# Performance work log

Hardware: AMD Instinct MI355X
Metric: run time of the kernel (lower is better)

The kernel has to match this reference:

```python
import jax, jax.numpy as jnp
import numpy as np

FACTOR = 2
EPS = 1e-5


def _layernorm_last(x, w, b):
    # LayerNorm over the last dim only (torch nn.LayerNorm(size) with int size)
    mu = jnp.mean(x, axis=-1, keepdims=True)
    var = jnp.var(x, axis=-1, keepdims=True)
    return (x - mu) * jax.lax.rsqrt(var + EPS) * w + b


def setup_inputs() -> dict:
    key = jax.random.key(0)
    ks = jax.random.split(key, 12)
    B, C, H, W = 8, 512, 128, 128
    C8 = C // 8
    S = (H // FACTOR)  # = 64, LayerNorm size
    x = jax.random.normal(ks[0], (B, C, H, W), jnp.float32)
    s = 1.0 / np.sqrt(C)
    wq = jax.random.normal(ks[1], (C8, C), jnp.float32) * s
    bq = jax.random.normal(ks[2], (C8,), jnp.float32) * 0.02
    wk = jax.random.normal(ks[3], (C8, C), jnp.float32) * s
    bk = jax.random.normal(ks[4], (C8,), jnp.float32) * 0.02
    wv = jax.random.normal(ks[5], (C, C), jnp.float32) * s
    bv = jax.random.normal(ks[6], (C,), jnp.float32) * 0.02
    gamma = jax.random.normal(ks[7], (1,), jnp.float32) * 0.1
    ln_in_w = 1.0 + 0.1 * jax.random.normal(ks[8], (S,), jnp.float32)
    ln_in_b = 0.1 * jax.random.normal(ks[9], (S,), jnp.float32)
    ln_out_w = 1.0 + 0.1 * jax.random.normal(ks[10], (S,), jnp.float32)
    ln_out_b = 0.1 * jax.random.normal(ks[11], (S,), jnp.float32)
    return {"x": x, "wq": wq, "bq": bq, "wk": wk, "bk": bk, "wv": wv, "bv": bv,
            "gamma": gamma, "ln_in_w": ln_in_w, "ln_in_b": ln_in_b,
            "ln_out_w": ln_out_w, "ln_out_b": ln_out_b}


def reference(x, wq, bq, wk, bk, wv, bv, gamma, ln_in_w, ln_in_b, ln_out_w, ln_out_b):
    B, C, H, W = x.shape
    f = FACTOR
    Hp, Wp = H // f, W // f
    N = Hp * Wp
    # AvgPool2d(factor)
    xp = x.reshape(B, C, Hp, f, Wp, f).mean(axis=(3, 5))
    # LayerNorm over last dim (width)
    xn = _layernorm_last(xp, ln_in_w, ln_in_b)
    # 1x1 conv projections (einsum over channels)
    q = jnp.einsum('oc,bchw->bohw', wq, xn) + bq[None, :, None, None]
    k = jnp.einsum('oc,bchw->bohw', wk, xn) + bk[None, :, None, None]
    v = jnp.einsum('oc,bchw->bohw', wv, xn) + bv[None, :, None, None]
    q = q.reshape(B, -1, N)  # (B, C/8, N)
    k = k.reshape(B, -1, N)
    v = v.reshape(B, C, N)
    # energy = Q^T K, no scale (as in source)
    energy = jnp.einsum('bcn,bcm->bnm', q, k)  # (B, N, N)
    att = jax.nn.softmax(energy, axis=-1)
    # out = V @ att^T : out[b,c,n] = sum_m v[b,c,m] * att[b,n,m]
    out = jnp.einsum('bcm,bnm->bcn', v, att).reshape(B, C, Hp, Wp)
    out = _layernorm_last(out, ln_out_w, ln_out_b)
    # F.interpolate(scale_factor=f) -> nearest upsample
    out = jnp.repeat(jnp.repeat(out, f, axis=2), f, axis=3)
    return gamma * out + x
```

## Files before the change

kernel.cpp:

```cpp
#include <hip/hip_runtime.h>
#include <hip/hip_bf16.h>
#include <stdint.h>

#define BB 8
#define CC 512
#define HH 128
#define WW 128
#define HP 64
#define NN 4096
#define C8 64
#define EPSF 1e-5f
#define LOG2E 1.4426950408889634f
#define SM_SHIFT 46.0f

typedef __attribute__((ext_vector_type(8))) short short8;
typedef __attribute__((ext_vector_type(4))) float f32x4;

__device__ __forceinline__ float bf2f(ushort u) {
    union { uint i; float f; } x; x.i = ((uint)u) << 16; return x.f;
}
__device__ __forceinline__ ushort f2bf(float f) {
    uint i = __float_as_uint(f);
    return (ushort)((i + 0x7FFFu + ((i >> 16) & 1u)) >> 16);
}
__device__ __forceinline__ uint cvt_pk_bf16(float lo, float hi) {
    uint r;
    asm("v_cvt_pk_bf16_f32 %0, %1, %2" : "=v"(r) : "v"(lo), "v"(hi));
    return r;
}

__global__ __launch_bounds__(256) void pool_ln_kernel(
    const float* __restrict__ x, const float* __restrict__ lw,
    const float* __restrict__ lb, ushort* __restrict__ xn)
{
    int wid = threadIdx.x >> 6, lane = threadIdx.x & 63;
    int row = blockIdx.x * 4 + wid;
    int h = row & 63;
    int bc = row >> 6;
    const float* r0 = x + ((size_t)bc * 128 + 2 * h) * 128;
    const float* r1 = r0 + 128;
    float2 a0 = ((const float2*)r0)[lane];
    float2 a1 = ((const float2*)r1)[lane];
    float p = 0.25f * (a0.x + a0.y + a1.x + a1.y);
    float s = p, sq = p * p;
    #pragma unroll
    for (int m = 1; m < 64; m <<= 1) {
        s  += __shfl_xor(s,  m, 64);
        sq += __shfl_xor(sq, m, 64);
    }
    float mu  = s * (1.f / 64.f);
    float var = sq * (1.f / 64.f) - mu * mu;
    float inv = rsqrtf(var + EPSF);
    float v = (p - mu) * inv * lw[lane] + lb[lane];
    xn[(size_t)bc * NN + h * 64 + lane] = f2bf(v);
}

__global__ __launch_bounds__(256) void qkv_kernel(
    const ushort* __restrict__ xn,
    const float* __restrict__ wq, const float* __restrict__ bq,
    const float* __restrict__ wk, const float* __restrict__ bk,
    const float* __restrict__ wv, const float* __restrict__ bv,
    ushort* __restrict__ qo, ushort* __restrict__ ko, ushort* __restrict__ vo)
{
    __shared__ __align__(16) ushort As[64][40];
    __shared__ __align__(16) ushort Bs[64][66];
    int b = blockIdx.z, mt = blockIdx.y;
    int n0 = blockIdx.x * 64;
    const float* W; const float* bias; ushort* outp;
    if (mt == 0)      { W = wq;                               bias = bq;              outp = qo + (size_t)b * C8 * NN; }
    else if (mt == 1) { W = wk;                               bias = bk;              outp = ko + (size_t)b * C8 * NN; }
    else              { W = wv + (size_t)(mt - 2) * 64 * 512; bias = bv + (mt - 2) * 64;
                        outp = vo + (size_t)b * CC * NN + (size_t)(mt - 2) * 64 * NN; }
    float mult = (mt == 0) ? LOG2E : 1.0f;
    const ushort* xb = xn + (size_t)b * CC * NN;
    int t = threadIdx.x;
    int lane = t & 63, wid = t >> 6;
    int wm = wid >> 1, wn = wid & 1;
    f32x4 acc[2][2] = {};

    for (int kc = 0; kc < 512; kc += 32) {
        {
            int row = t >> 2, k8 = (t & 3) * 8;
            const float* wp_ = &W[row * 512 + kc + k8];
            float4 f0 = *(const float4*)wp_;
            float4 f1 = *(const float4*)(wp_ + 4);
            ushort tmp[8] = { f2bf(f0.x * mult), f2bf(f0.y * mult), f2bf(f0.z * mult), f2bf(f0.w * mult),
                              f2bf(f1.x * mult), f2bf(f1.y * mult), f2bf(f1.z * mult), f2bf(f1.w * mult) };
            *(uint4*)&As[row][k8] = *(const uint4*)tmp;
        }
        {
            int c = t >> 3, n8 = (t & 7) * 8;
            uint4 v = *(const uint4*)&xb[(size_t)(kc + c) * NN + n0 + n8];
            const ushort* pv = (const ushort*)&v;
            #pragma unroll
            for (int e = 0; e < 8; e++) Bs[n8 + e][c] = pv[e];
        }
        __syncthreads();
        short8 a[2];
        #pragma unroll
        for (int fm = 0; fm < 2; fm++)
            a[fm] = *(const short8*)&As[wm * 32 + fm * 16 + (lane & 15)][(lane >> 4) * 8];
        short8 bb[2];
        #pragma unroll
        for (int fn = 0; fn < 2; fn++) {
            int col = wn * 32 + fn * 16 + (lane & 15);
            union { short8 v; uint u[4]; } bu;
            int c0 = (lane >> 4) * 8;
            #pragma unroll
            for (int p = 0; p < 4; p++)
                bu.u[p] = *(const uint*)&Bs[col][c0 + 2 * p];
            bb[fn] = bu.v;
        }
        #pragma unroll
        for (int fm = 0; fm < 2; fm++)
            #pragma unroll
            for (int fn = 0; fn < 2; fn++)
                acc[fm][fn] = __builtin_amdgcn_mfma_f32_16x16x32_bf16(a[fm], bb[fn], acc[fm][fn], 0, 0, 0);
        __syncthreads();
    }
    #pragma unroll
    for (int fm = 0; fm < 2; fm++) {
        #pragma unroll
        for (int fn = 0; fn < 2; fn++) {
            int col = n0 + wn * 32 + fn * 16 + (lane & 15);
            #pragma unroll
            for (int r = 0; r < 4; r++) {
                int orow = wm * 32 + fm * 16 + (lane >> 4) * 4 + r;
                outp[(size_t)orow * NN + col] = f2bf(acc[fm][fn][r] + bias[orow] * mult);
            }
        }
    }
}

__global__ __launch_bounds__(256, 4) void attn_kernel(
    const ushort* __restrict__ qg, const ushort* __restrict__ kg,
    const ushort* __restrict__ vg, const float* __restrict__ x,
    const float* __restrict__ gamma_p,
    const float* __restrict__ lnw_g, const float* __restrict__ lnb_g,
    float* __restrict__ out)
{
    __shared__ __align__(16) ushort KQ[2][4][64][16];
    __shared__ __align__(16) ushort Ps[2][64][72];
    __shared__ float row_l[64];
    __shared__ float lnw[64], lnb[64];

    int bid = blockIdx.x;
    int b  = bid & 7;
    int cq = (bid >> 3) & 3;
    int h  = bid >> 5;
    int t = threadIdx.x, wid = t >> 6, lane = t & 63;
    const ushort* qb = qg + (size_t)b * C8 * NN;
    const ushort* kb = kg + (size_t)b * C8 * NN;
    const ushort* vb = vg + (size_t)b * CC * NN;

    if (t < 64) { lnw[t] = lnw_g[t]; lnb[t] = lnb_g[t]; }

    int sc_ = t >> 2, sm16 = (t & 3) * 16;
    {
        *(uint4*)&KQ[1][t & 3][sc_][0] = *(const uint4*)&qb[(size_t)sc_ * NN + h * 64 + sm16];
        *(uint4*)&KQ[1][t & 3][sc_][8] = *(const uint4*)&qb[(size_t)sc_ * NN + h * 64 + sm16 + 8];
        *(uint4*)&KQ[0][t & 3][sc_][0] = *(const uint4*)&kb[(size_t)sc_ * NN + sm16];
        *(uint4*)&KQ[0][t & 3][sc_][8] = *(const uint4*)&kb[(size_t)sc_ * NN + sm16 + 8];
    }
    __syncthreads();

    uint trofs = 2u * ((uint)(lane & 15) + (((uint)lane >> 4) << 6));

    short8 qf[2];
    {
        uint qaddr = (uint)(uintptr_t)&KQ[1][wid][0][0] + trofs;
        union { short8 v; unsigned long long u[2]; } q0, q1;
        asm volatile("ds_read_b64_tr_b16 %0, %4\n"
                     "ds_read_b64_tr_b16 %1, %4 offset:512\n"
                     "ds_read_b64_tr_b16 %2, %4 offset:1024\n"
                     "ds_read_b64_tr_b16 %3, %4 offset:1536"
                     : "=&v"(q0.u[0]), "=&v"(q0.u[1]), "=&v"(q1.u[0]), "=&v"(q1.u[1])
                     : "v"(qaddr));
        asm volatile("s_waitcnt lgkmcnt(0)" ::: "memory");
        __builtin_amdgcn_sched_barrier(0);
        qf[0] = q0.v; qf[1] = q1.v;
    }
    __syncthreads();

    f32x4 acc[4][2] = {};
    float lsum = 0.f;
    int cbase = cq * 128 + wid * 32;
    int nrow = wid * 16 + (lane & 15);
    int mq4 = (lane >> 4) * 4;

    for (int mt = 0; mt < 64; mt++) {
        int cur = mt & 1, nxt = cur ^ 1;
        int m0 = mt * 64;
        int m0n = ((mt + 1) & 63) * 64;
        uint4 kp0 = *(const uint4*)&kb[(size_t)sc_ * NN + m0n + sm16];
        uint4 kp1 = *(const uint4*)&kb[(size_t)sc_ * NN + m0n + sm16 + 8];

        f32x4 sfT[4];
        #pragma unroll
        for (int fp = 0; fp < 2; fp++) {
            union { short8 v; unsigned long long u[2]; } ka[2], kc2[2];
            uint a0 = (uint)(uintptr_t)&KQ[cur][fp * 2][0][0] + trofs;
            uint a1 = (uint)(uintptr_t)&KQ[cur][fp * 2 + 1][0][0] + trofs;
            asm volatile("ds_read_b64_tr_b16 %0, %4\n"
                         "ds_read_b64_tr_b16 %1, %4 offset:512\n"
                         "ds_read_b64_tr_b16 %2, %4 offset:1024\n"
                         "ds_read_b64_tr_b16 %3, %4 offset:1536"
                         : "=&v"(ka[0].u[0]), "=&v"(ka[0].u[1]), "=&v"(ka[1].u[0]), "=&v"(ka[1].u[1])
                         : "v"(a0));
            asm volatile("ds_read_b64_tr_b16 %0, %4\n"
                         "ds_read_b64_tr_b16 %1, %4 offset:512\n"
                         "ds_read_b64_tr_b16 %2, %4 offset:1024\n"
                         "ds_read_b64_tr_b16 %3, %4 offset:1536"
                         : "=&v"(kc2[0].u[0]), "=&v"(kc2[0].u[1]), "=&v"(kc2[1].u[0]), "=&v"(kc2[1].u[1])
                         : "v"(a1));
            asm volatile("s_waitcnt lgkmcnt(0)" ::: "memory");
            __builtin_amdgcn_sched_barrier(0);
            f32x4 s0 = {}, s1 = {};
            s0 = __builtin_amdgcn_mfma_f32_16x16x32_bf16(ka[0].v,  qf[0], s0, 0, 0, 0);
            s0 = __builtin_amdgcn_mfma_f32_16x16x32_bf16(ka[1].v,  qf[1], s0, 0, 0, 0);
            s1 = __builtin_amdgcn_mfma_f32_16x16x32_bf16(kc2[0].v, qf[0], s1, 0, 0, 0);
            s1 = __builtin_amdgcn_mfma_f32_16x16x32_bf16(kc2[1].v, qf[1], s1, 0, 0, 0);
            sfT[fp * 2] = s0; sfT[fp * 2 + 1] = s1;
        }

        #pragma unroll
        for (int fn = 0; fn < 4; fn++) {
            float e0 = exp2f(sfT[fn][0] - SM_SHIFT);
            float e1 = exp2f(sfT[fn][1] - SM_SHIFT);
            float e2 = exp2f(sfT[fn][2] - SM_SHIFT);
            float e3 = exp2f(sfT[fn][3] - SM_SHIFT);
            lsum += (e0 + e1) + (e2 + e3);
            uint2 pk;
            pk.x = cvt_pk_bf16(e0, e1);
            pk.y = cvt_pk_bf16(e2, e3);
            *(uint2*)&Ps[cur][nrow][fn * 16 + mq4] = pk;
        }

        *(uint4*)&KQ[nxt][t & 3][sc_][0] = kp0;
        *(uint4*)&KQ[nxt][t & 3][sc_][8] = kp1;

        __syncthreads();

        #pragma unroll
        for (int ks = 0; ks < 2; ks++) {
            short8 pb[2];
            #pragma unroll
            for (int g = 0; g < 2; g++)
                pb[g] = *(const short8*)&vb[(size_t)(cbase + g * 16 + (lane & 15)) * NN
                                            + m0 + ks * 32 + (lane >> 4) * 8];
            short8 pa[4];
            #pragma unroll
            for (int f = 0; f < 4; f++)
                pa[f] = *(const short8*)&Ps[cur][f * 16 + (lane & 15)][ks * 32 + (lane >> 4) * 8];
            #pragma unroll
            for (int g = 0; g < 2; g++)
                #pragma unroll
                for (int f = 0; f < 4; f++)
                    acc[f][g] = __builtin_amdgcn_mfma_f32_16x16x32_bf16(pa[f], pb[g], acc[f][g], 0, 0, 0);
        }
    }

    lsum += __shfl_xor(lsum, 16, 64);
    lsum += __shfl_xor(lsum, 32, 64);
    if (lane < 16) row_l[wid * 16 + lane] = lsum;
    __syncthreads();

    float g = gamma_p[0];
    const float* xb2 = x + (size_t)b * CC * HH * WW;
    float* ob = out + (size_t)b * CC * HH * WW;
    float rl[4][4], lwv[4][4], lbv[4][4];
    #pragma unroll
    for (int fm = 0; fm < 4; fm++)
        #pragma unroll
        for (int r = 0; r < 4; r++) {
            int n = fm * 16 + (lane >> 4) * 4 + r;
            rl[fm][r] = 1.f / row_l[n];
            lwv[fm][r] = lnw[n]; lbv[fm][r] = lnb[n];
        }
    #pragma unroll
    for (int fc = 0; fc < 2; fc++) {
        int c = cbase + fc * 16 + (lane & 15);
        float vv[4][4];
        float vsum = 0.f, vsq = 0.f;
        #pragma unroll
        for (int fm = 0; fm < 4; fm++)
            #pragma unroll
            for (int r = 0; r < 4; r++) {
                float v = acc[fm][fc][r] * rl[fm][r];
                vv[fm][r] = v; vsum += v; vsq += v * v;
            }
        vsum += __shfl_xor(vsum, 16, 64); vsum += __shfl_xor(vsum, 32, 64);
        vsq  += __shfl_xor(vsq,  16, 64); vsq  += __shfl_xor(vsq,  32, 64);
        float mu  = vsum * (1.f / 64.f);
        float var = vsq * (1.f / 64.f) - mu * mu;
        float inv = rsqrtf(var + EPSF);
        const float* xrow = xb2 + (size_t)c * HH * WW + (2 * h) * WW;
        float*       orow = ob  + (size_t)c * HH * WW + (2 * h) * WW;
        #pragma unroll
        for (int fm = 0; fm < 4; fm++) {
            int nbase = fm * 16 + (lane >> 4) * 4;
            float nv[4];
            #pragma unroll
            for (int r = 0; r < 4; r++)
                nv[r] = g * ((vv[fm][r] - mu) * inv * lwv[fm][r] + lbv[fm][r]);
            #pragma unroll
            for (int dh = 0; dh < 2; dh++) {
                float4 xv0 = *(const float4*)&xrow[dh * WW + 2 * nbase];
                float4 xv1 = *(const float4*)&xrow[dh * WW + 2 * nbase + 4];
                float4 o0, o1;
                o0.x = nv[0] + xv0.x; o0.y = nv[0] + xv0.y;
                o0.z = nv[1] + xv0.z; o0.w = nv[1] + xv0.w;
                o1.x = nv[2] + xv1.x; o1.y = nv[2] + xv1.y;
                o1.z = nv[3] + xv1.z; o1.w = nv[3] + xv1.w;
                *(float4*)&orow[dh * WW + 2 * nbase]     = o0;
                *(float4*)&orow[dh * WW + 2 * nbase + 4] = o1;
            }
        }
    }
}

extern "C" void kernel_launch(void* const* d_in, const int* in_sizes, int n_in,
                              void* d_out, int out_size, void* d_ws, size_t ws_size,
                              hipStream_t stream)
{
    (void)in_sizes; (void)n_in; (void)out_size; (void)ws_size;
    const float* x    = (const float*)d_in[0];
    const float* wq   = (const float*)d_in[1];
    const float* bq   = (const float*)d_in[2];
    const float* wk   = (const float*)d_in[3];
    const float* bk   = (const float*)d_in[4];
    const float* wv   = (const float*)d_in[5];
    const float* bv   = (const float*)d_in[6];
    const float* gam  = (const float*)d_in[7];
    const float* lniw = (const float*)d_in[8];
    const float* lnib = (const float*)d_in[9];
    const float* lnow = (const float*)d_in[10];
    const float* lnob = (const float*)d_in[11];
    float* out = (float*)d_out;

    char* ws = (char*)d_ws;
    ushort* xn = (ushort*)(ws);
    ushort* q  = (ushort*)(ws + 33554432u);
    ushort* k  = (ushort*)(ws + 37748736u);
    ushort* v  = (ushort*)(ws + 41943040u);

    pool_ln_kernel<<<65536, 256, 0, stream>>>(x, lniw, lnib, xn);
    qkv_kernel<<<dim3(64, 10, 8), 256, 0, stream>>>(xn, wq, bq, wk, bk, wv, bv, q, k, v);
    attn_kernel<<<2048, 256, 0, stream>>>(q, k, v, x, gam, lnow, lnob, out);
}
```

Before: 489.8 us.

## Store Q/K transposed and load K fragments directly from global, skew PV stage

The QKV kernel now writes Q and K in token-major (N x 64) layout, so the attention kernel can load MFMA fragments for Q and K straight from global memory. This drops the shared-memory K staging buffer and the transpose reads. The P·V product is also deferred by one iteration, so it runs on the previous tile's P while the current scores are computed, which leaves one barrier per step. The cost is more global K loads per wave, since each wave now reads the whole K tile itself.

```diff
diff --git a/kernel.cpp b/kernel.cpp
--- a/kernel.cpp
+++ b/kernel.cpp
@@ -60,17 +60,16 @@
     const float* __restrict__ wq, const float* __restrict__ bq,
     const float* __restrict__ wk, const float* __restrict__ bk,
     const float* __restrict__ wv, const float* __restrict__ bv,
-    ushort* __restrict__ qo, ushort* __restrict__ ko, ushort* __restrict__ vo)
+    ushort* __restrict__ qt, ushort* __restrict__ kt, ushort* __restrict__ vo)
 {
     __shared__ __align__(16) ushort As[64][40];
     __shared__ __align__(16) ushort Bs[64][66];
     int b = blockIdx.z, mt = blockIdx.y;
     int n0 = blockIdx.x * 64;
-    const float* W; const float* bias; ushort* outp;
-    if (mt == 0)      { W = wq;                               bias = bq;              outp = qo + (size_t)b * C8 * NN; }
-    else if (mt == 1) { W = wk;                               bias = bk;              outp = ko + (size_t)b * C8 * NN; }
-    else              { W = wv + (size_t)(mt - 2) * 64 * 512; bias = bv + (mt - 2) * 64;
-                        outp = vo + (size_t)b * CC * NN + (size_t)(mt - 2) * 64 * NN; }
+    const float* W; const float* bias;
+    if (mt == 0)      { W = wq;                               bias = bq; }
+    else if (mt == 1) { W = wk;                               bias = bk; }
+    else              { W = wv + (size_t)(mt - 2) * 64 * 512; bias = bv + (mt - 2) * 64; }
     float mult = (mt == 0) ? LOG2E : 1.0f;
     const ushort* xb = xn + (size_t)b * CC * NN;
     int t = threadIdx.x;
@@ -118,28 +117,45 @@
                 acc[fm][fn] = __builtin_amdgcn_mfma_f32_16x16x32_bf16(a[fm], bb[fn], acc[fm][fn], 0, 0, 0);
         __syncthreads();
     }
-    #pragma unroll
-    for (int fm = 0; fm < 2; fm++) {
-        #pragma unroll
-        for (int fn = 0; fn < 2; fn++) {
-            int col = n0 + wn * 32 + fn * 16 + (lane & 15);
-            #pragma unroll
-            for (int r = 0; r < 4; r++) {
-                int orow = wm * 32 + fm * 16 + (lane >> 4) * 4 + r;
-                outp[(size_t)orow * NN + col] = f2bf(acc[fm][fn][r] + bias[orow] * mult);
+    if (mt <= 1) {
+        ushort* ot = ((mt == 0) ? qt : kt) + (size_t)b * NN * 64;
+        #pragma unroll
+        for (int fm = 0; fm < 2; fm++) {
+            #pragma unroll
+            for (int fn = 0; fn < 2; fn++) {
+                int col = n0 + wn * 32 + fn * 16 + (lane & 15);
+                int c0  = wm * 32 + fm * 16 + (lane >> 4) * 4;
+                ushort tmp[4];
+                #pragma unroll
+                for (int r = 0; r < 4; r++)
+                    tmp[r] = f2bf(acc[fm][fn][r] + bias[c0 + r] * mult);
+                *(uint2*)&ot[(size_t)col * 64 + c0] = *(const uint2*)tmp;
+            }
+        }
+    } else {
+        ushort* outp = vo + (size_t)b * CC * NN + (size_t)(mt - 2) * 64 * NN;
+        #pragma unroll
+        for (int fm = 0; fm < 2; fm++) {
+            #pragma unroll
+            for (int fn = 0; fn < 2; fn++) {
+                int col = n0 + wn * 32 + fn * 16 + (lane & 15);
+                #pragma unroll
+                for (int r = 0; r < 4; r++) {
+                    int orow = wm * 32 + fm * 16 + (lane >> 4) * 4 + r;
+                    outp[(size_t)orow * NN + col] = f2bf(acc[fm][fn][r] + bias[orow]);
+                }
             }
         }
     }
 }
 
 __global__ __launch_bounds__(256, 4) void attn_kernel(
-    const ushort* __restrict__ qg, const ushort* __restrict__ kg,
+    const ushort* __restrict__ qt, const ushort* __restrict__ ktg,
     const ushort* __restrict__ vg, const float* __restrict__ x,
     const float* __restrict__ gamma_p,
     const float* __restrict__ lnw_g, const float* __restrict__ lnb_g,
     float* __restrict__ out)
 {
-    __shared__ __align__(16) ushort KQ[2][4][64][16];
     __shared__ __align__(16) ushort Ps[2][64][72];
     __shared__ float row_l[64];
     __shared__ float lnw[64], lnb[64];
@@ -149,78 +165,63 @@
     int cq = (bid >> 3) & 3;
     int h  = bid >> 5;
     int t = threadIdx.x, wid = t >> 6, lane = t & 63;
-    const ushort* qb = qg + (size_t)b * C8 * NN;
-    const ushort* kb = kg + (size_t)b * C8 * NN;
-    const ushort* vb = vg + (size_t)b * CC * NN;
+    int l15 = lane & 15, hig = lane >> 4;
+    const ushort* ktb = ktg + (size_t)b * NN * 64;
+    const ushort* vb  = vg  + (size_t)b * CC * NN;
 
     if (t < 64) { lnw[t] = lnw_g[t]; lnb[t] = lnb_g[t]; }
 
-    int sc_ = t >> 2, sm16 = (t & 3) * 16;
-    {
-        *(uint4*)&KQ[1][t & 3][sc_][0] = *(const uint4*)&qb[(size_t)sc_ * NN + h * 64 + sm16];
-        *(uint4*)&KQ[1][t & 3][sc_][8] = *(const uint4*)&qb[(size_t)sc_ * NN + h * 64 + sm16 + 8];
-        *(uint4*)&KQ[0][t & 3][sc_][0] = *(const uint4*)&kb[(size_t)sc_ * NN + sm16];
-        *(uint4*)&KQ[0][t & 3][sc_][8] = *(const uint4*)&kb[(size_t)sc_ * NN + sm16 + 8];
-    }
-    __syncthreads();
-
-    uint trofs = 2u * ((uint)(lane & 15) + (((uint)lane >> 4) << 6));
-
-    short8 qf[2];
-    {
-        uint qaddr = (uint)(uintptr_t)&KQ[1][wid][0][0] + trofs;
-        union { short8 v; unsigned long long u[2]; } q0, q1;
-        asm volatile("ds_read_b64_tr_b16 %0, %4\n"
-                     "ds_read_b64_tr_b16 %1, %4 offset:512\n"
-                     "ds_read_b64_tr_b16 %2, %4 offset:1024\n"
-                     "ds_read_b64_tr_b16 %3, %4 offset:1536"
-                     : "=&v"(q0.u[0]), "=&v"(q0.u[1]), "=&v"(q1.u[0]), "=&v"(q1.u[1])
-                     : "v"(qaddr));
-        asm volatile("s_waitcnt lgkmcnt(0)" ::: "memory");
-        __builtin_amdgcn_sched_barrier(0);
-        qf[0] = q0.v; qf[1] = q1.v;
-    }
-    __syncthreads();
+    const ushort* qrow = qt + (size_t)b * NN * 64 + (size_t)(h * 64 + wid * 16 + l15) * 64;
+    short8 qf0 = *(const short8*)&qrow[hig * 8];
+    short8 qf1 = *(const short8*)&qrow[32 + hig * 8];
 
     f32x4 acc[4][2] = {};
     float lsum = 0.f;
     int cbase = cq * 128 + wid * 32;
-    int nrow = wid * 16 + (lane & 15);
-    int mq4 = (lane >> 4) * 4;
-
-    for (int mt = 0; mt < 64; mt++) {
-        int cur = mt & 1, nxt = cur ^ 1;
-        int m0 = mt * 64;
-        int m0n = ((mt + 1) & 63) * 64;
-        uint4 kp0 = *(const uint4*)&kb[(size_t)sc_ * NN + m0n + sm16];
-        uint4 kp1 = *(const uint4*)&kb[(size_t)sc_ * NN + m0n + sm16 + 8];
+    int nrow = wid * 16 + l15;
+    int mq4 = hig * 4;
+    size_t ktvoff = (size_t)(l15 * 64 + hig * 8);
+
+    __syncthreads();
+
+    for (int mt2 = 0; mt2 < 64; mt2++) {
+        int cur = mt2 & 1;
+        const ushort* kp = ktb + (size_t)(mt2 * 64) * 64 + ktvoff;
+        short8 ktf[8];
+        #pragma unroll
+        for (int mf = 0; mf < 4; mf++) {
+            ktf[mf * 2]     = *(const short8*)(kp + (size_t)mf * 1024);
+            ktf[mf * 2 + 1] = *(const short8*)(kp + (size_t)mf * 1024 + 32);
+        }
+
+        if (mt2 > 0) {
+            int m0 = (mt2 - 1) * 64, pbuf = cur ^ 1;
+            #pragma unroll
+            for (int ks = 0; ks < 2; ks++) {
+                short8 pb[2];
+                #pragma unroll
+                for (int g = 0; g < 2; g++)
+                    pb[g] = *(const short8*)&vb[(size_t)(cbase + g * 16 + l15) * NN
+                                                + m0 + ks * 32 + hig * 8];
+                short8 pa[4];
+                #pragma unroll
+                for (int f = 0; f < 4; f++)
+                    pa[f] = *(const short8*)&Ps[pbuf][f * 16 + l15][ks * 32 + hig * 8];
+                #pragma unroll
+                for (int g = 0; g < 2; g++)
+                    #pragma unroll
+                    for (int f = 0; f < 4; f++)
+                        acc[f][g] = __builtin_amdgcn_mfma_f32_16x16x32_bf16(pa[f], pb[g], acc[f][g], 0, 0, 0);
+            }
+        }
 
         f32x4 sfT[4];
         #pragma unroll
-        for (int fp = 0; fp < 2; fp++) {
-            union { short8 v; unsigned long long u[2]; } ka[2], kc2[2];
-            uint a0 = (uint)(uintptr_t)&KQ[cur][fp * 2][0][0] + trofs;
-            uint a1 = (uint)(uintptr_t)&KQ[cur][fp * 2 + 1][0][0] + trofs;
-            asm volatile("ds_read_b64_tr_b16 %0, %4\n"
-                         "ds_read_b64_tr_b16 %1, %4 offset:512\n"
-                         "ds_read_b64_tr_b16 %2, %4 offset:1024\n"
-                         "ds_read_b64_tr_b16 %3, %4 offset:1536"
-                         : "=&v"(ka[0].u[0]), "=&v"(ka[0].u[1]), "=&v"(ka[1].u[0]), "=&v"(ka[1].u[1])
-                         : "v"(a0));
-            asm volatile("ds_read_b64_tr_b16 %0, %4\n"
-                         "ds_read_b64_tr_b16 %1, %4 offset:512\n"
-                         "ds_read_b64_tr_b16 %2, %4 offset:1024\n"
-                         "ds_read_b64_tr_b16 %3, %4 offset:1536"
-                         : "=&v"(kc2[0].u[0]), "=&v"(kc2[0].u[1]), "=&v"(kc2[1].u[0]), "=&v"(kc2[1].u[1])
-                         : "v"(a1));
-            asm volatile("s_waitcnt lgkmcnt(0)" ::: "memory");
-            __builtin_amdgcn_sched_barrier(0);
-            f32x4 s0 = {}, s1 = {};
-            s0 = __builtin_amdgcn_mfma_f32_16x16x32_bf16(ka[0].v,  qf[0], s0, 0, 0, 0);
-            s0 = __builtin_amdgcn_mfma_f32_16x16x32_bf16(ka[1].v,  qf[1], s0, 0, 0, 0);
-            s1 = __builtin_amdgcn_mfma_f32_16x16x32_bf16(kc2[0].v, qf[0], s1, 0, 0, 0);
-            s1 = __builtin_amdgcn_mfma_f32_16x16x32_bf16(kc2[1].v, qf[1], s1, 0, 0, 0);
-            sfT[fp * 2] = s0; sfT[fp * 2 + 1] = s1;
+        for (int mf = 0; mf < 4; mf++) {
+            f32x4 s = {};
+            s = __builtin_amdgcn_mfma_f32_16x16x32_bf16(ktf[mf * 2],     qf0, s, 0, 0, 0);
+            s = __builtin_amdgcn_mfma_f32_16x16x32_bf16(ktf[mf * 2 + 1], qf1, s, 0, 0, 0);
+            sfT[mf] = s;
         }
 
         #pragma unroll
@@ -235,23 +236,21 @@
             pk.y = cvt_pk_bf16(e2, e3);
             *(uint2*)&Ps[cur][nrow][fn * 16 + mq4] = pk;
         }
-
-        *(uint4*)&KQ[nxt][t & 3][sc_][0] = kp0;
-        *(uint4*)&KQ[nxt][t & 3][sc_][8] = kp1;
-
         __syncthreads();
-
+    }
+    {
+        int m0 = 63 * 64;
         #pragma unroll
         for (int ks = 0; ks < 2; ks++) {
             short8 pb[2];
             #pragma unroll
             for (int g = 0; g < 2; g++)
-                pb[g] = *(const short8*)&vb[(size_t)(cbase + g * 16 + (lane & 15)) * NN
-                                            + m0 + ks * 32 + (lane >> 4) * 8];
+                pb[g] = *(const short8*)&vb[(size_t)(cbase + g * 16 + l15) * NN
+                                            + m0 + ks * 32 + hig * 8];
             short8 pa[4];
             #pragma unroll
             for (int f = 0; f < 4; f++)
-                pa[f] = *(const short8*)&Ps[cur][f * 16 + (lane & 15)][ks * 32 + (lane >> 4) * 8];
+                pa[f] = *(const short8*)&Ps[1][f * 16 + l15][ks * 32 + hig * 8];
             #pragma unroll
             for (int g = 0; g < 2; g++)
                 #pragma unroll
@@ -273,13 +272,13 @@
     for (int fm = 0; fm < 4; fm++)
         #pragma unroll
         for (int r = 0; r < 4; r++) {
-            int n = fm * 16 + (lane >> 4) * 4 + r;
+            int n = fm * 16 + hig * 4 + r;
             rl[fm][r] = 1.f / row_l[n];
             lwv[fm][r] = lnw[n]; lbv[fm][r] = lnb[n];
         }
     #pragma unroll
     for (int fc = 0; fc < 2; fc++) {
-        int c = cbase + fc * 16 + (lane & 15);
+        int c = cbase + fc * 16 + l15;
         float vv[4][4];
         float vsum = 0.f, vsq = 0.f;
         #pragma unroll
@@ -298,7 +297,7 @@
         float*       orow = ob  + (size_t)c * HH * WW + (2 * h) * WW;
         #pragma unroll
         for (int fm = 0; fm < 4; fm++) {
-            int nbase = fm * 16 + (lane >> 4) * 4;
+            int nbase = fm * 16 + hig * 4;
             float nv[4];
             #pragma unroll
             for (int r = 0; r < 4; r++)
@@ -340,11 +339,11 @@
 
     char* ws = (char*)d_ws;
     ushort* xn = (ushort*)(ws);
-    ushort* q  = (ushort*)(ws + 33554432u);
-    ushort* k  = (ushort*)(ws + 37748736u);
+    ushort* qt = (ushort*)(ws + 33554432u);
+    ushort* kt = (ushort*)(ws + 37748736u);
     ushort* v  = (ushort*)(ws + 41943040u);
 
     pool_ln_kernel<<<65536, 256, 0, stream>>>(x, lniw, lnib, xn);
-    qkv_kernel<<<dim3(64, 10, 8), 256, 0, stream>>>(xn, wq, bq, wk, bk, wv, bv, q, k, v);
-    attn_kernel<<<2048, 256, 0, stream>>>(q, k, v, x, gam, lnow, lnob, out);
-}
+    qkv_kernel<<<dim3(64, 10, 8), 256, 0, stream>>>(xn, wq, bq, wk, bk, wv, bv, qt, kt, v);
+    attn_kernel<<<2048, 256, 0, stream>>>(qt, kt, v, x, gam, lnow, lnob, out);
+}
```

After: 893.3 us. 1.82x slower.
